# Kernel optimization log

Measured on AMD Instinct MI355X. Metric: run time of the kernel, lower is better.

## Reference

```python
import jax, jax.numpy as jnp
import numpy as np

HIDDEN = 4096
NUM_HEADS = 32
NUM_KV_HEADS = 8
HEAD_DIM = 128
EPS = 1e-6
ROPE_THETA = 1000000.0


def setup_inputs() -> dict:
    key = jax.random.key(0)
    ks = jax.random.split(key, 6)
    T = 2048
    qkv_out = (NUM_HEADS + 2 * NUM_KV_HEADS) * HEAD_DIM
    scale_in = 1.0 / np.sqrt(HIDDEN)
    return {
        "positions": jnp.arange(T, dtype=jnp.int64 if jax.config.jax_enable_x64 else jnp.int32),
        "hidden_states": jax.random.normal(ks[0], (T, HIDDEN), dtype=jnp.float32),
        "w_qkv": jax.random.normal(ks[1], (HIDDEN, qkv_out), dtype=jnp.float32) * scale_in,
        "q_norm_w": jnp.ones((HEAD_DIM,), dtype=jnp.float32),
        "k_norm_w": jnp.ones((HEAD_DIM,), dtype=jnp.float32),
        "w_o": jax.random.normal(ks[2], (NUM_HEADS * HEAD_DIM, HIDDEN), dtype=jnp.float32) * (1.0 / np.sqrt(NUM_HEADS * HEAD_DIM)),
    }


def _rms_norm(x, w):
    # per-head RMSNorm over last dim, computed in fp32
    xf = x.astype(jnp.float32)
    var = jnp.mean(xf * xf, axis=-1, keepdims=True)
    return (xf * jax.lax.rsqrt(var + EPS) * w).astype(x.dtype)


def _rope(x, positions):
    # neox-style RoPE over full head_dim
    half = HEAD_DIM // 2
    inv_freq = 1.0 / (ROPE_THETA ** (jnp.arange(0, half, dtype=jnp.float32) / half))
    ang = positions.astype(jnp.float32)[:, None] * inv_freq  # [T, half]
    cos = jnp.cos(ang)[:, None, :]  # [T, 1, half]
    sin = jnp.sin(ang)[:, None, :]
    x1, x2 = x[..., :half], x[..., half:]
    return jnp.concatenate([x1 * cos - x2 * sin, x2 * cos + x1 * sin], axis=-1).astype(x.dtype)


def reference(positions, hidden_states, w_qkv, q_norm_w, k_norm_w, w_o):
    T = hidden_states.shape[0]
    G = NUM_HEADS // NUM_KV_HEADS  # GQA group size
    qkv = hidden_states @ w_qkv  # [T, (nh+2*nkv)*hd]
    q_size = NUM_HEADS * HEAD_DIM
    kv_size = NUM_KV_HEADS * HEAD_DIM
    q = qkv[:, :q_size].reshape(T, NUM_HEADS, HEAD_DIM)
    k = qkv[:, q_size:q_size + kv_size].reshape(T, NUM_KV_HEADS, HEAD_DIM)
    v = qkv[:, q_size + kv_size:].reshape(T, NUM_KV_HEADS, HEAD_DIM)

    q = _rms_norm(q, q_norm_w)
    k = _rms_norm(k, k_norm_w)
    q = _rope(q, positions)
    k = _rope(k, positions)

    scaling = HEAD_DIM ** -0.5
    qg = q.reshape(T, NUM_KV_HEADS, G, HEAD_DIM)
    # scores: [nkv, G, T_q, T_kv]
    scores = jnp.einsum('tkgd,skd->kgts', qg, k) * scaling
    causal = positions[:, None] >= positions[None, :]  # [T, T]
    scores = jnp.where(causal[None, None], scores, jnp.float32(-1e30))
    probs = jax.nn.softmax(scores, axis=-1)
    out = jnp.einsum('kgts,skd->tkgd', probs, v).reshape(T, NUM_HEADS * HEAD_DIM)
    return out @ w_o
```

## Files before the change

kernel.cpp:

```cpp
#include <hip/hip_runtime.h>

#define T_SEQ 2048
#define HID   4096
#define NQH   32
#define NKVH  8
#define HD    128
#define QKV_N 6144

typedef __attribute__((ext_vector_type(8))) __bf16 bf16x8;
typedef __attribute__((ext_vector_type(4))) float floatx4;

static __device__ __forceinline__ unsigned short f2bf(float f) {
  union { float f; unsigned u; } v; v.f = f;
  unsigned r = v.u + 0x7fffu + ((v.u >> 16) & 1u);
  return (unsigned short)(r >> 16);
}
static __device__ __forceinline__ float bf2f(unsigned short u) {
  union { unsigned u; float f; } v; v.u = ((unsigned)u) << 16;
  return v.f;
}

static __device__ __forceinline__ void gld_lds16(const unsigned short* g, unsigned short* l) {
  __builtin_amdgcn_global_load_lds(
      (const __attribute__((address_space(1))) unsigned int*)g,
      (__attribute__((address_space(3))) unsigned int*)l, 16, 0, 0);
}

__global__ __launch_bounds__(256) void cast_f32_bf16(
    const float* __restrict__ in, unsigned short* __restrict__ out) {
  int i = (blockIdx.x * 256 + threadIdx.x) * 4;
  float4 v = *(const float4*)(in + i);
  ushort4 o;
  o.x = f2bf(v.x); o.y = f2bf(v.y); o.z = f2bf(v.z); o.w = f2bf(v.w);
  *(ushort4*)(out + i) = o;
}

__global__ __launch_bounds__(256) void transpose_f32_bf16(
    const float* __restrict__ in, unsigned short* __restrict__ out,
    int R, int C) {
  __shared__ unsigned short tile[64][65];
  const int c0 = blockIdx.x * 64, r0 = blockIdx.y * 64;
  const int tr = threadIdx.x >> 4;
  const int tc = (threadIdx.x & 15) * 4;
#pragma unroll
  for (int p = 0; p < 4; p++) {
    int r = tr + p * 16;
    float4 v = *(const float4*)(in + (size_t)(r0 + r) * C + c0 + tc);
    tile[r][tc] = f2bf(v.x); tile[r][tc + 1] = f2bf(v.y);
    tile[r][tc + 2] = f2bf(v.z); tile[r][tc + 3] = f2bf(v.w);
  }
  __syncthreads();
#pragma unroll
  for (int p = 0; p < 4; p++) {
    int c = tr + p * 16;
    ushort4 o;
    o.x = tile[tc][c]; o.y = tile[tc + 1][c]; o.z = tile[tc + 2][c]; o.w = tile[tc + 3][c];
    *(ushort4*)(out + (size_t)(c0 + c) * R + r0 + tc) = o;
  }
}

__global__ __launch_bounds__(256) void gemm_bt(
    const unsigned short* __restrict__ A, const unsigned short* __restrict__ Bt,
    float* __restrict__ Cf, unsigned short* __restrict__ Cb,
    int M, int N, int K) {
  __shared__ unsigned short As[128][32];
  __shared__ unsigned short Bs[128][32];
  const int tid = threadIdx.x, lane = tid & 63, wv = tid >> 6;
  const int m0 = blockIdx.y * 128, n0 = blockIdx.x * 128;
  const int wm = (wv >> 1) * 64, wn = (wv & 1) * 64;
  const int quad = lane >> 4, mc = lane & 15;
  const int srow = wv * 32 + (lane >> 2);
  const int scol = (lane & 3) * 8;
  const unsigned short* gA = A + (size_t)(m0 + srow) * K + scol;
  const unsigned short* gB = Bt + (size_t)(n0 + srow) * K + scol;
  unsigned short* lA0 = &As[wv * 32][0];
  unsigned short* lA1 = &As[wv * 32 + 16][0];
  unsigned short* lB0 = &Bs[wv * 32][0];
  unsigned short* lB1 = &Bs[wv * 32 + 16][0];
  floatx4 acc[4][4] = {};
  for (int k0 = 0; k0 < K; k0 += 32) {
    gld_lds16(gA + k0, lA0);
    gld_lds16(gA + k0 + (size_t)16 * K, lA1);
    gld_lds16(gB + k0, lB0);
    gld_lds16(gB + k0 + (size_t)16 * K, lB1);
    __syncthreads();
    bf16x8 af[4], bfr[4];
#pragma unroll
    for (int i = 0; i < 4; i++) af[i] = *(const bf16x8*)(&As[wm + i * 16 + mc][quad * 8]);
#pragma unroll
    for (int j = 0; j < 4; j++) bfr[j] = *(const bf16x8*)(&Bs[wn + j * 16 + mc][quad * 8]);
#pragma unroll
    for (int i = 0; i < 4; i++)
#pragma unroll
      for (int j = 0; j < 4; j++)
        acc[i][j] = __builtin_amdgcn_mfma_f32_16x16x32_bf16(af[i], bfr[j], acc[i][j], 0, 0, 0);
    __syncthreads();
  }
#pragma unroll
  for (int i = 0; i < 4; i++)
#pragma unroll
    for (int j = 0; j < 4; j++)
#pragma unroll
      for (int r = 0; r < 4; r++) {
        int row = m0 + wm + i * 16 + quad * 4 + r;
        int col = n0 + wn + j * 16 + mc;
        if (Cf) Cf[(size_t)row * N + col] = acc[i][j][r];
        else    Cb[(size_t)row * N + col] = f2bf(acc[i][j][r]);
      }
}

__global__ __launch_bounds__(64) void normrope_kernel(
    const unsigned short* __restrict__ qkv,
    const float* __restrict__ qw, const float* __restrict__ kw,
    unsigned short* __restrict__ qout, unsigned short* __restrict__ kout,
    unsigned short* __restrict__ vt) {
  const int t = blockIdx.x, hh = blockIdx.y, ln = threadIdx.x;
  const unsigned short* x = qkv + (size_t)t * QKV_N + hh * HD;
  if (hh >= NQH + NKVH) {
    int kvh = hh - (NQH + NKVH);
    vt[((size_t)kvh * HD + ln) * T_SEQ + t] = x[ln];
    vt[((size_t)kvh * HD + ln + 64) * T_SEQ + t] = x[ln + 64];
    return;
  }
  float x0 = bf2f(x[ln]), x1 = bf2f(x[ln + 64]);
  float ss = x0 * x0 + x1 * x1;
#pragma unroll
  for (int off = 32; off > 0; off >>= 1) ss += __shfl_xor(ss, off, 64);
  float rinv = rsqrtf(ss * (1.0f / 128.0f) + 1e-6f);
  const float* w = (hh < NQH) ? qw : kw;
  float y0 = x0 * rinv * w[ln];
  float y1 = x1 * rinv * w[ln + 64];
  float pos = (float)t;
  float inv_freq = expf(((float)ln) * (-13.815510557964274f / 64.0f));
  float ang = pos * inv_freq;
  float s, c;
  sincosf(ang, &s, &c);
  float o0 = y0 * c - y1 * s;
  float o1 = y1 * c + y0 * s;
  if (hh < NQH) {
    qout[((size_t)t * NQH + hh) * HD + ln] = f2bf(o0);
    qout[((size_t)t * NQH + hh) * HD + ln + 64] = f2bf(o1);
  } else {
    int kh = hh - NQH;
    kout[((size_t)t * NKVH + kh) * HD + ln] = f2bf(o0);
    kout[((size_t)t * NKVH + kh) * HD + ln + 64] = f2bf(o1);
  }
}

__global__ __launch_bounds__(256, 2) void attn_kernel(
    const unsigned short* __restrict__ qb, const unsigned short* __restrict__ kb,
    const unsigned short* __restrict__ vt, unsigned short* __restrict__ aout) {
  __shared__ unsigned short smem[27136];
  unsigned short* Ks = smem;
  unsigned short* Vs = smem + 8704;
  unsigned short* Ps = smem + 17920;
  const int bx = blockIdx.x;
  const int kvh = blockIdx.y;
  const int qt = (kvh < 4) ? bx : (63 - bx);
  const int q0 = qt * 32;
  const int tid = threadIdx.x, lane = tid & 63, wv = tid >> 6;
  const int h = kvh * 4 + wv;
  const int quad = lane >> 4, mc = lane & 15;
  const float c2 = 0.1275356394f;
  const __bf16 one = (__bf16)1.0f;
  const bf16x8 ones = {one, one, one, one, one, one, one, one};
  bf16x8 qf[2][4];
#pragma unroll
  for (int mi = 0; mi < 2; mi++)
#pragma unroll
    for (int kc = 0; kc < 4; kc++)
      qf[mi][kc] = *(const bf16x8*)(
          qb + ((size_t)(q0 + mi * 16 + mc) * NQH + h) * HD + kc * 32 + quad * 8);

  const unsigned short* kbase = kb + ((size_t)(tid >> 4) * NKVH + kvh) * HD + (tid & 15) * 8;
  const unsigned short* vbase = vt + ((size_t)kvh * HD + (tid >> 3)) * T_SEQ + (tid & 7) * 8;
  unsigned short* kdst = Ks + (tid >> 4) * 136 + (tid & 15) * 8;
  unsigned short* vdst = Vs + (tid >> 3) * 72 + (tid & 7) * 8;
  const size_t kstep = (size_t)16 * (NKVH * HD);
  const size_t vstep = (size_t)32 * T_SEQ;

  floatx4 O[2][8] = {};
  floatx4 lac[2] = {};
  const int ntiles = (qt >> 1) + 1;

  uint4 kr0 = *(const uint4*)(kbase);
  uint4 kr1 = *(const uint4*)(kbase + kstep);
  uint4 kr2 = *(const uint4*)(kbase + 2 * kstep);
  uint4 kr3 = *(const uint4*)(kbase + 3 * kstep);
  uint4 vr0 = *(const uint4*)(vbase);
  uint4 vr1 = *(const uint4*)(vbase + vstep);
  uint4 vr2 = *(const uint4*)(vbase + 2 * vstep);
  uint4 vr3 = *(const uint4*)(vbase + 3 * vstep);

  for (int it = 0; it < ntiles; it++) {
    const int s0 = it * 64;
    __syncthreads();
    *(uint4*)(kdst)                = kr0;
    *(uint4*)(kdst + 16 * 136)     = kr1;
    *(uint4*)(kdst + 32 * 136)     = kr2;
    *(uint4*)(kdst + 48 * 136)     = kr3;
    *(uint4*)(vdst)                = vr0;
    *(uint4*)(vdst + 32 * 72)      = vr1;
    *(uint4*)(vdst + 64 * 72)      = vr2;
    *(uint4*)(vdst + 96 * 72)      = vr3;
    if (it + 1 < ntiles) {
      const int s0n = s0 + 64;
      const unsigned short* kn = kbase + (size_t)s0n * (NKVH * HD);
      const unsigned short* vn = vbase + s0n;
      kr0 = *(const uint4*)(kn);
      kr1 = *(const uint4*)(kn + kstep);
      kr2 = *(const uint4*)(kn + 2 * kstep);
      kr3 = *(const uint4*)(kn + 3 * kstep);
      vr0 = *(const uint4*)(vn);
      vr1 = *(const uint4*)(vn + vstep);
      vr2 = *(const uint4*)(vn + 2 * vstep);
      vr3 = *(const uint4*)(vn + 3 * vstep);
    }
    __syncthreads();
#pragma unroll
    for (int jt = 0; jt < 4; jt++) {
      bf16x8 bfr[4];
#pragma unroll
      for (int kc = 0; kc < 4; kc++)
        bfr[kc] = *(const bf16x8*)(Ks + (jt * 16 + mc) * 136 + kc * 32 + quad * 8);
#pragma unroll
      for (int mi = 0; mi < 2; mi++) {
        floatx4 acc = {};
        __builtin_amdgcn_s_setprio(1);
#pragma unroll
        for (int kc = 0; kc < 4; kc++)
          acc = __builtin_amdgcn_mfma_f32_16x16x32_bf16(qf[mi][kc], bfr[kc], acc, 0, 0, 0);
        __builtin_amdgcn_s_setprio(0);
        int qrow = q0 + mi * 16 + quad * 4;
        int scol = s0 + jt * 16 + mc;
#pragma unroll
        for (int r = 0; r < 4; r++) {
          float p = (scol <= qrow + r) ? exp2f(acc[r] * c2) : 0.f;
          Ps[(size_t)(wv * 32 + mi * 16 + quad * 4 + r) * 72 + jt * 16 + mc] = f2bf(p);
        }
      }
    }
    bf16x8 pa[2][2];
#pragma unroll
    for (int mi = 0; mi < 2; mi++)
#pragma unroll
      for (int kb2 = 0; kb2 < 2; kb2++)
        pa[mi][kb2] = *(const bf16x8*)(Ps + (size_t)(wv * 32 + mi * 16 + mc) * 72 + kb2 * 32 + quad * 8);
    __builtin_amdgcn_s_setprio(1);
#pragma unroll
    for (int mi = 0; mi < 2; mi++) {
      lac[mi] = __builtin_amdgcn_mfma_f32_16x16x32_bf16(pa[mi][0], ones, lac[mi], 0, 0, 0);
      lac[mi] = __builtin_amdgcn_mfma_f32_16x16x32_bf16(pa[mi][1], ones, lac[mi], 0, 0, 0);
    }
    __builtin_amdgcn_s_setprio(0);
#pragma unroll
    for (int jd = 0; jd < 8; jd++) {
      bf16x8 vb0 = *(const bf16x8*)(Vs + (jd * 16 + mc) * 72 + quad * 8);
      bf16x8 vb1 = *(const bf16x8*)(Vs + (jd * 16 + mc) * 72 + 32 + quad * 8);
      __builtin_amdgcn_s_setprio(1);
#pragma unroll
      for (int mi = 0; mi < 2; mi++) {
        O[mi][jd] = __builtin_amdgcn_mfma_f32_16x16x32_bf16(pa[mi][0], vb0, O[mi][jd], 0, 0, 0);
        O[mi][jd] = __builtin_amdgcn_mfma_f32_16x16x32_bf16(pa[mi][1], vb1, O[mi][jd], 0, 0, 0);
      }
      __builtin_amdgcn_s_setprio(0);
    }
  }
  __syncthreads();
  float rl[2][4];
#pragma unroll
  for (int mi = 0; mi < 2; mi++)
#pragma unroll
    for (int r = 0; r < 4; r++) rl[mi][r] = 1.0f / lac[mi][r];
#pragma unroll
  for (int mi = 0; mi < 2; mi++)
#pragma unroll
    for (int jd = 0; jd < 8; jd++)
#pragma unroll
      for (int r = 0; r < 4; r++)
        smem[(size_t)(wv * 32 + mi * 16 + quad * 4 + r) * 128 + jd * 16 + mc] =
            f2bf(O[mi][jd][r] * rl[mi][r]);
  __syncthreads();
  const int rr = tid >> 1;
  const int cb = (tid & 1) * 64;
  const size_t gbase = (size_t)(q0 + (rr & 31)) * (NQH * HD) + (kvh * 4 + (rr >> 5)) * HD + cb;
#pragma unroll
  for (int i = 0; i < 8; i++) {
    uint4 v = *(const uint4*)(smem + (size_t)rr * 128 + cb + i * 8);
    *(uint4*)(aout + gbase + i * 8) = v;
  }
}

extern "C" void kernel_launch(void* const* d_in, const int* in_sizes, int n_in,
                              void* d_out, int out_size, void* d_ws, size_t ws_size,
                              hipStream_t stream) {
  const float* hidden    = (const float*)d_in[1];
  const float* w_qkv     = (const float*)d_in[2];
  const float* q_norm    = (const float*)d_in[3];
  const float* k_norm    = (const float*)d_in[4];
  const float* w_o       = (const float*)d_in[5];
  float* out             = (float*)d_out;
  char* ws = (char*)d_ws;
  unsigned short* wqkv_t   = (unsigned short*)(ws);
  unsigned short* q_bf     = (unsigned short*)(ws);
  unsigned short* k_bf     = (unsigned short*)(ws + 16777216);
  unsigned short* v_t      = (unsigned short*)(ws + 20971520);
  unsigned short* attn     = (unsigned short*)(ws + 25165824);
  unsigned short* qkv_bf   = (unsigned short*)(ws + 50331648);
  unsigned short* wo_t     = (unsigned short*)(ws + 50331648);
  unsigned short* hidden_b = (unsigned short*)(ws + 75497472);

  cast_f32_bf16<<<dim3((T_SEQ * HID) / 1024), 256, 0, stream>>>(hidden, hidden_b);
  transpose_f32_bf16<<<dim3(QKV_N / 64, HID / 64), 256, 0, stream>>>(w_qkv, wqkv_t, HID, QKV_N);
  gemm_bt<<<dim3(QKV_N / 128, T_SEQ / 128), 256, 0, stream>>>(
      hidden_b, wqkv_t, nullptr, qkv_bf, T_SEQ, QKV_N, HID);
  normrope_kernel<<<dim3(T_SEQ, NQH + 2 * NKVH), 64, 0, stream>>>(
      qkv_bf, q_norm, k_norm, q_bf, k_bf, v_t);
  transpose_f32_bf16<<<dim3(HID / 64, HID / 64), 256, 0, stream>>>(w_o, wo_t, HID, HID);
  attn_kernel<<<dim3(T_SEQ / 32, NKVH), 256, 0, stream>>>(q_bf, k_bf, v_t, attn);
  gemm_bt<<<dim3(HID / 128, T_SEQ / 128), 256, 0, stream>>>(
      attn, wo_t, out, nullptr, T_SEQ, HID, HID);
}
```

Before: 577.9 us.

## Rewrite GEMM with 256-row tiles, double-buffered LDS prefetch and swizzled layout

Replaces the simple 128x128 single-buffered GEMM with a templated 512-thread kernel that uses 256xBN tiles, a K-step of 64, and double-buffered LDS. Loads for the next tile are issued between MFMA phases. An XOR swizzle on the LDS layout avoids bank conflicts, and s_setprio is raised around the MFMA bursts. The aim is to hide global load latency, raise arithmetic intensity, and cut the number of barriers. In exchange it needs much more LDS and many more accumulator registers, which may limit occupancy.

```diff
diff --git a/kernel.cpp b/kernel.cpp
--- a/kernel.cpp
+++ b/kernel.cpp
@@ -59,51 +59,106 @@
   }
 }
 
-__global__ __launch_bounds__(256) void gemm_bt(
+template <int BN>
+__global__ __launch_bounds__(512, 2) void gemm_bt2(
     const unsigned short* __restrict__ A, const unsigned short* __restrict__ Bt,
     float* __restrict__ Cf, unsigned short* __restrict__ Cb,
     int M, int N, int K) {
-  __shared__ unsigned short As[128][32];
-  __shared__ unsigned short Bs[128][32];
+  constexpr int NJ = BN / 64;
+  __shared__ unsigned short lds[2 * 16384 + 2 * BN * 64];
   const int tid = threadIdx.x, lane = tid & 63, wv = tid >> 6;
-  const int m0 = blockIdx.y * 128, n0 = blockIdx.x * 128;
-  const int wm = (wv >> 1) * 64, wn = (wv & 1) * 64;
   const int quad = lane >> 4, mc = lane & 15;
-  const int srow = wv * 32 + (lane >> 2);
-  const int scol = (lane & 3) * 8;
-  const unsigned short* gA = A + (size_t)(m0 + srow) * K + scol;
-  const unsigned short* gB = Bt + (size_t)(n0 + srow) * K + scol;
-  unsigned short* lA0 = &As[wv * 32][0];
-  unsigned short* lA1 = &As[wv * 32 + 16][0];
-  unsigned short* lB0 = &Bs[wv * 32][0];
-  unsigned short* lB1 = &Bs[wv * 32 + 16][0];
-  floatx4 acc[4][4] = {};
-  for (int k0 = 0; k0 < K; k0 += 32) {
-    gld_lds16(gA + k0, lA0);
-    gld_lds16(gA + k0 + (size_t)16 * K, lA1);
-    gld_lds16(gB + k0, lB0);
-    gld_lds16(gB + k0 + (size_t)16 * K, lB1);
-    __syncthreads();
-    bf16x8 af[4], bfr[4];
-#pragma unroll
-    for (int i = 0; i < 4; i++) af[i] = *(const bf16x8*)(&As[wm + i * 16 + mc][quad * 8]);
-#pragma unroll
-    for (int j = 0; j < 4; j++) bfr[j] = *(const bf16x8*)(&Bs[wn + j * 16 + mc][quad * 8]);
-#pragma unroll
-    for (int i = 0; i < 4; i++)
-#pragma unroll
-      for (int j = 0; j < 4; j++)
-        acc[i][j] = __builtin_amdgcn_mfma_f32_16x16x32_bf16(af[i], bfr[j], acc[i][j], 0, 0, 0);
-    __syncthreads();
-  }
-#pragma unroll
-  for (int i = 0; i < 4; i++)
-#pragma unroll
-    for (int j = 0; j < 4; j++)
-#pragma unroll
-      for (int r = 0; r < 4; r++) {
-        int row = m0 + wm + i * 16 + quad * 4 + r;
-        int col = n0 + wn + j * 16 + mc;
+  const int wr = wv >> 2, wc = wv & 3;
+  const int m0 = blockIdx.y * 256, n0 = blockIdx.x * BN;
+  const int NK = K >> 6;
+  unsigned short* curA = lds;
+  unsigned short* nxtA = lds + 16384;
+  unsigned short* curB = lds + 32768;
+  unsigned short* nxtB = lds + 32768 + BN * 64;
+  const int arow = tid >> 3;
+  const int sl8 = (((tid & 7) ^ (arow & 7)) << 3);
+  const unsigned short* gA = A + (size_t)(m0 + arow) * K + sl8;
+  const unsigned short* gB = Bt + (size_t)(n0 + arow) * K + sl8;
+  const int ldst = wv * 512;
+  const size_t kW = (size_t)64 * K;
+  const int s0 = ((quad ^ (mc & 7)) << 3);
+  const int s1 = (((4 + quad) ^ (mc & 7)) << 3);
+  floatx4 acc[8][NJ] = {};
+#pragma unroll
+  for (int i = 0; i < NJ; ++i) gld_lds16(gB + (size_t)i * kW, curB + i * 4096 + ldst);
+#pragma unroll
+  for (int i = 0; i < 4; ++i)  gld_lds16(gA + (size_t)i * kW, curA + i * 4096 + ldst);
+
+#define GPHASE(I0)                                                                   \
+  do {                                                                               \
+    const unsigned short* p0_ = curA + (wr * 128 + (I0) * 16 + mc) * 64;             \
+    const unsigned short* p1_ = p0_ + 16 * 64;                                       \
+    bf16x8 a00 = *(const bf16x8*)(p0_ + s0), a01 = *(const bf16x8*)(p0_ + s1);       \
+    bf16x8 a10 = *(const bf16x8*)(p1_ + s0), a11 = *(const bf16x8*)(p1_ + s1);       \
+    __builtin_amdgcn_s_setprio(1);                                                   \
+    _Pragma("unroll")                                                                \
+    for (int j = 0; j < NJ; ++j) {                                                   \
+      acc[(I0)][j] = __builtin_amdgcn_mfma_f32_16x16x32_bf16(a00, bfr[j][0], acc[(I0)][j], 0, 0, 0);     \
+      acc[(I0)][j] = __builtin_amdgcn_mfma_f32_16x16x32_bf16(a01, bfr[j][1], acc[(I0)][j], 0, 0, 0);     \
+      acc[(I0)+1][j] = __builtin_amdgcn_mfma_f32_16x16x32_bf16(a10, bfr[j][0], acc[(I0)+1][j], 0, 0, 0); \
+      acc[(I0)+1][j] = __builtin_amdgcn_mfma_f32_16x16x32_bf16(a11, bfr[j][1], acc[(I0)+1][j], 0, 0, 0); \
+    }                                                                                \
+    __builtin_amdgcn_s_setprio(0);                                                   \
+  } while (0)
+
+  for (int kt = 0; kt < NK; ++kt) {
+    asm volatile("s_waitcnt vmcnt(0)\n\ts_barrier" ::: "memory");
+    const bool pre = (kt + 1 < NK);
+    const unsigned short* gAn = gA + (size_t)(kt + 1) * 64;
+    const unsigned short* gBn = gB + (size_t)(kt + 1) * 64;
+    if (pre) { gld_lds16(gBn, nxtB + ldst); gld_lds16(gBn + kW, nxtB + 4096 + ldst); }
+    bf16x8 bfr[NJ][2];
+#pragma unroll
+    for (int j = 0; j < NJ; ++j) {
+      const unsigned short* p = curB + (wc * (16 * NJ) + j * 16 + mc) * 64;
+      bfr[j][0] = *(const bf16x8*)(p + s0);
+      bfr[j][1] = *(const bf16x8*)(p + s1);
+    }
+    GPHASE(0);
+    if (pre) {
+      if constexpr (NJ == 4) {
+        gld_lds16(gBn + 2 * kW, nxtB + 8192 + ldst);
+        gld_lds16(gBn + 3 * kW, nxtB + 12288 + ldst);
+      } else {
+        gld_lds16(gAn, nxtA + ldst);
+        gld_lds16(gAn + kW, nxtA + 4096 + ldst);
+      }
+    }
+    GPHASE(2);
+    if (pre) {
+      if constexpr (NJ == 4) {
+        gld_lds16(gAn, nxtA + ldst);
+        gld_lds16(gAn + kW, nxtA + 4096 + ldst);
+      } else {
+        gld_lds16(gAn + 2 * kW, nxtA + 8192 + ldst);
+        gld_lds16(gAn + 3 * kW, nxtA + 12288 + ldst);
+      }
+    }
+    GPHASE(4);
+    if (pre) {
+      if constexpr (NJ == 4) {
+        gld_lds16(gAn + 2 * kW, nxtA + 8192 + ldst);
+        gld_lds16(gAn + 3 * kW, nxtA + 12288 + ldst);
+      }
+    }
+    GPHASE(6);
+    { unsigned short* t = curA; curA = nxtA; nxtA = t;
+      t = curB; curB = nxtB; nxtB = t; }
+  }
+#undef GPHASE
+#pragma unroll
+  for (int i = 0; i < 8; ++i)
+#pragma unroll
+    for (int j = 0; j < NJ; ++j)
+#pragma unroll
+      for (int r = 0; r < 4; ++r) {
+        int row = m0 + wr * 128 + i * 16 + quad * 4 + r;
+        int col = n0 + wc * (16 * NJ) + j * 16 + mc;
         if (Cf) Cf[(size_t)row * N + col] = acc[i][j][r];
         else    Cb[(size_t)row * N + col] = f2bf(acc[i][j][r]);
       }
@@ -312,12 +367,12 @@
 
   cast_f32_bf16<<<dim3((T_SEQ * HID) / 1024), 256, 0, stream>>>(hidden, hidden_b);
   transpose_f32_bf16<<<dim3(QKV_N / 64, HID / 64), 256, 0, stream>>>(w_qkv, wqkv_t, HID, QKV_N);
-  gemm_bt<<<dim3(QKV_N / 128, T_SEQ / 128), 256, 0, stream>>>(
+  gemm_bt2<256><<<dim3(QKV_N / 256, T_SEQ / 256), 512, 0, stream>>>(
       hidden_b, wqkv_t, nullptr, qkv_bf, T_SEQ, QKV_N, HID);
   normrope_kernel<<<dim3(T_SEQ, NQH + 2 * NKVH), 64, 0, stream>>>(
       qkv_bf, q_norm, k_norm, q_bf, k_bf, v_t);
   transpose_f32_bf16<<<dim3(HID / 64, HID / 64), 256, 0, stream>>>(w_o, wo_t, HID, HID);
   attn_kernel<<<dim3(T_SEQ / 32, NKVH), 256, 0, stream>>>(q_bf, k_bf, v_t, attn);
-  gemm_bt<<<dim3(HID / 128, T_SEQ / 128), 256, 0, stream>>>(
+  gemm_bt2<128><<<dim3(HID / 128, T_SEQ / 256), 512, 0, stream>>>(
       attn, wo_t, out, nullptr, T_SEQ, HID, HID);
 }
```

Measured after the change: 520.3 us. 10.0% less time.
